# Optimization experiments

Measured on AMD Instinct MI355X. Metric: run time of the kernel, lower is better.

Reference implementation:

```python
import jax, jax.numpy as jnp
import numpy as np

B, H, W, D, R = 2, 128, 128, 128, 3   # batch, volume dims, number of SMV radii
LAM = 1e-3                            # Tikhonov term keeping the CG operator PD
EPS = 1e-12
TRUN = 10                             # truncated CG iteration count


def setup_inputs():
    key = jax.random.key(0)
    ks = jax.random.split(key, 4)
    x = jax.random.normal(ks[0], (B, H, W, D, 1), jnp.float32)
    x1 = (jax.random.uniform(ks[1], (B, H, W, D, R)) > 0.2).astype(jnp.float32)  # binary SMV masks per radius
    x3 = jax.random.uniform(ks[2], (B, H, W, D, 1), jnp.float32)        # voxelwise data weight
    init_x = jnp.zeros((B, H, W, D, 1), jnp.float32)                    # CG warm start
    smv = jax.random.uniform(ks[3], (R, H, W, D), jnp.float32)          # SMV kernels in k-space (real)
    return {"x": x, "x1": x1, "x3": x3, "init_x": init_x, "smv": smv, "trun": TRUN}


def _cg_solve(x, x1, x3, init_x, smv, trun):
    # Solve (S^H M S + lam I) u = S^H M (w3 * x) with truncated CG,
    # where S applies per-radius SMV convolution via 3D FFT and M = diag(masks).
    xv = x[..., 0]            # [B,H,W,D]
    x0 = init_x[..., 0]       # [B,H,W,D]
    w3 = x3[..., 0]           # [B,H,W,D]
    m = jnp.moveaxis(x1, -1, 1)  # [B,R,H,W,D]

    def smv_fwd(v):           # [B,H,W,D] -> [B,R,H,W,D]
        Fv = jnp.fft.fftn(v, axes=(1, 2, 3))
        return jnp.real(jnp.fft.ifftn(smv[None] * Fv[:, None], axes=(2, 3, 4)))

    def smv_adj(u):           # [B,R,H,W,D] -> [B,H,W,D] (smv real => self-adjoint kernel)
        Fu = (smv[None] * jnp.fft.fftn(u, axes=(2, 3, 4))).sum(axis=1)
        return jnp.real(jnp.fft.ifftn(Fu, axes=(1, 2, 3)))

    def A(v):
        return smv_adj(m * smv_fwd(v)) + LAM * v

    def pdot(a, b):           # per-batch inner product -> [B]
        return jnp.sum(a * b, axis=(1, 2, 3))

    b = smv_adj(m * (w3 * xv)[:, None])
    r0 = b - A(x0)

    def step(carry, _):
        xk, r, p, rs = carry
        Ap = A(p)
        alpha = (rs / (pdot(p, Ap) + EPS))[:, None, None, None]
        xk = xk + alpha * p
        r = r - alpha * Ap
        rs_new = pdot(r, r)
        beta = (rs_new / (rs + EPS))[:, None, None, None]
        p = r + beta * p
        return (xk, r, p, rs_new), None

    (xk, _, _, _), _ = jax.lax.scan(step, (x0, r0, r0, pdot(r0, r0)), None, length=trun)
    return xk[..., None]      # [B,H,W,D,1]


def reference(x, x1, x3, init_x, smv, trun):
    return _cg_solve(x, x1, x3, init_x, smv, trun)
```

## Files before the change

### kernel.cpp

```cpp
#include <hip/hip_runtime.h>

#define PI_F 3.14159265358979323846f
constexpr int VOL = 1 << 21;
constexpr float LAMBDA = 1e-3f;
constexpr int TRUNC = 10;
constexpr int LDSB = 128 * 129 * 8;

__device__ __forceinline__ float2 cmulf(float2 a, float2 b) {
    return make_float2(a.x * b.x - a.y * b.y, a.x * b.y + a.y * b.x);
}
__device__ __forceinline__ float2 cmulcf(float2 a, float2 b) {
    return make_float2(a.x * b.x + a.y * b.y, a.y * b.x - a.x * b.y);
}

template <int M>
__device__ __forceinline__ float shx(float v) {
    if constexpr (M == 1)
        return __int_as_float(__builtin_amdgcn_mov_dpp(__float_as_int(v), 0xB1, 0xF, 0xF, true));
    else if constexpr (M == 2)
        return __int_as_float(__builtin_amdgcn_mov_dpp(__float_as_int(v), 0x4E, 0xF, 0xF, true));
    else if constexpr (M == 4 || M == 8 || M == 16)
        return __int_as_float(__builtin_amdgcn_ds_swizzle(__float_as_int(v), (M << 10) | 0x1F));
    else
        return __shfl_xor(v, 32, 64);
}

__device__ __forceinline__ void plswap32(float2& a, float2& b) {
#if __has_builtin(__builtin_amdgcn_permlane32_swap)
    {
        auto rx = __builtin_amdgcn_permlane32_swap(__float_as_uint(a.x), __float_as_uint(b.x), false, false);
        a.x = __uint_as_float(rx[0]);
        b.x = __uint_as_float(rx[1]);
        auto ry = __builtin_amdgcn_permlane32_swap(__float_as_uint(a.y), __float_as_uint(b.y), false, false);
        a.y = __uint_as_float(ry[0]);
        b.y = __uint_as_float(ry[1]);
    }
#else
    {
        bool hi = (threadIdx.x & 32) != 0;
        float pax = __shfl_xor(a.x, 32, 64), pay = __shfl_xor(a.y, 32, 64);
        float pbx = __shfl_xor(b.x, 32, 64), pby = __shfl_xor(b.y, 32, 64);
        float2 na = hi ? make_float2(pbx, pby) : a;
        float2 nb = hi ? b : make_float2(pax, pay);
        a = na; b = nb;
    }
#endif
}

template <int NL>
__device__ __forceinline__ void fwd_pl32(float2 v[NL], float2 w32) {
#pragma unroll
    for (int l = 0; l < NL; l += 2) {
        plswap32(v[l], v[l + 1]);
        float2 s = make_float2(v[l].x + v[l + 1].x, v[l].y + v[l + 1].y);
        float2 d = cmulf(make_float2(v[l].x - v[l + 1].x, v[l].y - v[l + 1].y), w32);
        plswap32(s, d);
        v[l] = s;
        v[l + 1] = d;
    }
}

template <int NL>
__device__ __forceinline__ void inv_pl32(float2 v[NL], float2 w32) {
#pragma unroll
    for (int l = 0; l < NL; l += 2) {
        plswap32(v[l], v[l + 1]);
        float2 t = cmulcf(v[l + 1], w32);
        float2 s = make_float2(v[l].x + t.x, v[l].y + t.y);
        float2 d = make_float2(v[l].x - t.x, v[l].y - t.y);
        plswap32(s, d);
        v[l] = s;
        v[l + 1] = d;
    }
}

__device__ __forceinline__ void twinit2(int lane, float2 wl[6], float sg[6],
                                        float2& tw6, float2& w32) {
#pragma unroll
    for (int s = 0; s < 6; s++) {
        int m = 1 << s;
        bool hi = (lane & m) != 0;
        float ang = -PI_F * (float)(lane & (m - 1)) / (float)m;
        float sn, cs;
        __sincosf(ang, &sn, &cs);
        wl[s] = hi ? make_float2(cs, sn) : make_float2(1.f, 0.f);
        sg[s] = hi ? -1.f : 1.f;
    }
    float sn, cs;
    __sincosf(-PI_F * (float)(lane & 31) / 32.f, &sn, &cs);
    w32 = make_float2(cs, sn);
    __sincosf(-PI_F * (float)lane / 64.f, &sn, &cs);
    tw6 = make_float2(cs, sn);
}

template <int NL, int M, int S>
__device__ __forceinline__ void fwd_stage(float2 v0[NL], float2 v1[NL],
                                          const float2 wl[6], const float sg[6]) {
    const float2 w = wl[S];
    const float s = sg[S];
#pragma unroll
    for (int l = 0; l < NL; l++) {
        float2 p0 = make_float2(shx<M>(v0[l].x), shx<M>(v0[l].y));
        float2 p1 = make_float2(shx<M>(v1[l].x), shx<M>(v1[l].y));
        float2 t0 = make_float2(fmaf(v0[l].x, s, p0.x), fmaf(v0[l].y, s, p0.y));
        float2 t1 = make_float2(fmaf(v1[l].x, s, p1.x), fmaf(v1[l].y, s, p1.y));
        v0[l] = cmulf(t0, w);
        v1[l] = cmulf(t1, w);
    }
}

template <int NL, int M, int S>
__device__ __forceinline__ void inv_stage(float2 v0[NL], float2 v1[NL],
                                          const float2 wl[6], const float sg[6]) {
    const float2 w = wl[S];
    const float s = sg[S];
#pragma unroll
    for (int l = 0; l < NL; l++) {
        float2 u0 = cmulcf(v0[l], w);
        float2 u1 = cmulcf(v1[l], w);
        float2 p0 = make_float2(shx<M>(u0.x), shx<M>(u0.y));
        float2 p1 = make_float2(shx<M>(u1.x), shx<M>(u1.y));
        v0[l] = make_float2(fmaf(u0.x, s, p0.x), fmaf(u0.y, s, p0.y));
        v1[l] = make_float2(fmaf(u1.x, s, p1.x), fmaf(u1.y, s, p1.y));
    }
}

template <int NL>
__device__ __forceinline__ void fft_fwd_b(float2 v0[NL], float2 v1[NL],
                                          const float2 wl[6], const float sg[6],
                                          float2 tw6, float2 w32) {
#pragma unroll
    for (int l = 0; l < NL; l++) {
        float2 a = v0[l], b = v1[l];
        v0[l] = make_float2(a.x + b.x, a.y + b.y);
        v1[l] = cmulf(make_float2(a.x - b.x, a.y - b.y), tw6);
    }
    fwd_pl32<NL>(v0, w32);
    fwd_pl32<NL>(v1, w32);
    fwd_stage<NL, 16, 4>(v0, v1, wl, sg);
    fwd_stage<NL, 8, 3>(v0, v1, wl, sg);
    fwd_stage<NL, 4, 2>(v0, v1, wl, sg);
    fwd_stage<NL, 2, 1>(v0, v1, wl, sg);
    fwd_stage<NL, 1, 0>(v0, v1, wl, sg);
}

template <int NL>
__device__ __forceinline__ void fft_inv_b(float2 v0[NL], float2 v1[NL],
                                          const float2 wl[6], const float sg[6],
                                          float2 tw6, float2 w32) {
    inv_stage<NL, 1, 0>(v0, v1, wl, sg);
    inv_stage<NL, 2, 1>(v0, v1, wl, sg);
    inv_stage<NL, 4, 2>(v0, v1, wl, sg);
    inv_stage<NL, 8, 3>(v0, v1, wl, sg);
    inv_stage<NL, 16, 4>(v0, v1, wl, sg);
    inv_pl32<NL>(v0, w32);
    inv_pl32<NL>(v1, w32);
#pragma unroll
    for (int l = 0; l < NL; l++) {
        float2 t = cmulcf(v1[l], tw6);
        float2 n0 = make_float2(v0[l].x + t.x, v0[l].y + t.y);
        v1[l] = make_float2(v0[l].x - t.x, v0[l].y - t.y);
        v0[l] = n0;
    }
}

__device__ __forceinline__ void cg_ab(const float* scal, int i, float aP[2], float bI[2]) {
#pragma unroll
    for (int b = 0; b < 2; b++) {
        double rs = (double)scal[b], rsp = rs, a = 0.0;
        for (int k = 0; k < i; k++) {
            double pap = (double)scal[2 + 6 * k + b];
            double rap = (double)scal[4 + 6 * k + b];
            double apap = (double)scal[6 + 6 * k + b];
            a = rs / (pap + 1e-12);
            rsp = rs;
            rs = rs - 2.0 * a * rap + a * a * apap;
        }
        aP[b] = (float)a;
        bI[b] = (float)(rs / (rsp + 1e-12));
    }
}

#define PF_FWD   1
#define PF_PRE   2
#define PF_UPDP  4
#define PF_MASK  8
#define PF_LAM  16
#define PF_BOUT 32

#define LD(w_, d_) lds[(w_) * 129 + (d_)]

template <int MODE>
__global__ __launch_bounds__(1024) void k_plane(const float2* src,
                                                float2* dst,
                                                const unsigned char* __restrict__ mpk,
                                                const float2* pr,
                                                float2* pw,
                                                float2* xp,
                                                const float2* ap,
                                                float2* rw,
                                                float* __restrict__ scal, int iter) {
    extern __shared__ float2 lds[];
    __shared__ float red[6][16];
    const int t = threadIdx.x, lane = t & 63, wv = t >> 6;
    const int plane = blockIdx.x & 127;
    const int rr = blockIdx.x >> 7;
    const size_t pb = (size_t)plane * 16384;
    const size_t vb = (size_t)rr * VOL;
    float2 wl[6]; float sg[6]; float2 tw6; float2 w32;
    twinit2(lane, wl, sg, tw6, w32);

    if (MODE & PF_FWD) {
        float aP[2] = {0.f, 0.f}, bI[2] = {0.f, 0.f};
        if (MODE & PF_UPDP) cg_ab(scal, iter, aP, bI);
        float2 v0[8], v1[8];
#pragma unroll
        for (int l = 0; l < 8; l++) {
            int w = wv * 8 + l;
            size_t g = pb + (size_t)w * 128;
            if (MODE & PF_UPDP) {
                float2 r0 = rw[g + lane], r1 = rw[g + lane + 64];
                float2 p0 = pr[g + lane], p1 = pr[g + lane + 64];
                float2 A0 = ap[g + lane], A1 = ap[g + lane + 64];
                float2 X0 = xp[g + lane], X1 = xp[g + lane + 64];
                X0.x += aP[0] * p0.x; X0.y += aP[1] * p0.y;
                X1.x += aP[0] * p1.x; X1.y += aP[1] * p1.y;
                r0.x -= aP[0] * A0.x; r0.y -= aP[1] * A0.y;
                r1.x -= aP[0] * A1.x; r1.y -= aP[1] * A1.y;
                xp[g + lane] = X0; xp[g + lane + 64] = X1;
                rw[g + lane] = r0; rw[g + lane + 64] = r1;
                v0[l] = make_float2(r0.x + bI[0] * p0.x, r0.y + bI[1] * p0.y);
                v1[l] = make_float2(r1.x + bI[0] * p1.x, r1.y + bI[1] * p1.y);
                pw[g + lane] = v0[l]; pw[g + lane + 64] = v1[l];
            } else {
                v0[l] = src[g + lane];
                v1[l] = src[g + lane + 64];
                if (MODE & PF_PRE) {
                    unsigned m0 = mpk[g + lane], m1 = mpk[g + lane + 64];
                    v0[l].x *= (float)((m0 >> rr) & 1);
                    v0[l].y *= (float)((m0 >> (3 + rr)) & 1);
                    v1[l].x *= (float)((m1 >> rr) & 1);
                    v1[l].y *= (float)((m1 >> (3 + rr)) & 1);
                }
            }
        }
        fft_fwd_b<8>(v0, v1, wl, sg, tw6, w32);
#pragma unroll
        for (int l = 0; l < 8; l++) {
            int w = wv * 8 + l;
            LD(w, lane) = v0[l];
            LD(w, lane + 64) = v1[l];
        }
        __syncthreads();
#pragma unroll
        for (int l = 0; l < 8; l++) {
            int d = wv * 8 + l;
            v0[l] = LD(lane, d); v1[l] = LD(lane + 64, d);
        }
        fft_fwd_b<8>(v0, v1, wl, sg, tw6, w32);
#pragma unroll
        for (int l = 0; l < 8; l++) {
            int d = wv * 8 + l;
            LD(lane, d) = v0[l]; LD(lane + 64, d) = v1[l];
        }
        __syncthreads();
        float2* dv = dst + ((MODE & PF_PRE) ? vb : 0);
#pragma unroll
        for (int i = 0; i < 8; i++) {
            int e = t + 1024 * i;
            int w = e >> 6, d = (e & 63) * 2;
            float2 a = LD(w, d), c = LD(w, d + 1);
            *(float4*)&dv[pb + (size_t)w * 128 + d] = make_float4(a.x, a.y, c.x, c.y);
        }
    } else {
        unsigned mb0[8], mb1[8];
        if (MODE & PF_MASK) {
#pragma unroll
            for (int l = 0; l < 8; l++) {
                size_t g = pb + (size_t)(wv * 8 + l) * 128;
                mb0[l] = mpk[g + lane];
                mb1[l] = mpk[g + lane + 64];
            }
        }
        const float2* sv = src + ((MODE & PF_MASK) ? vb : 0);
#pragma unroll
        for (int i = 0; i < 8; i++) {
            int e = t + 1024 * i;
            int w = e >> 6, d = (e & 63) * 2;
            float4 f = *(const float4*)&sv[pb + (size_t)w * 128 + d];
            LD(w, d) = make_float2(f.x, f.y);
            LD(w, d + 1) = make_float2(f.z, f.w);
        }
        __syncthreads();
        float2 v0[8], v1[8];
#pragma unroll
        for (int l = 0; l < 8; l++) {
            int d = wv * 8 + l;
            v0[l] = LD(lane, d); v1[l] = LD(lane + 64, d);
        }
        fft_inv_b<8>(v0, v1, wl, sg, tw6, w32);
#pragma unroll
        for (int l = 0; l < 8; l++) {
            int d = wv * 8 + l;
            LD(lane, d) = v0[l]; LD(lane + 64, d) = v1[l];
        }
        __syncthreads();
#pragma unroll
        for (int l = 0; l < 8; l++) {
            int w = wv * 8 + l;
            v0[l] = LD(w, lane); v1[l] = LD(w, lane + 64);
        }
        fft_inv_b<8>(v0, v1, wl, sg, tw6, w32);
        float dd[6] = {0.f, 0.f, 0.f, 0.f, 0.f, 0.f};
        if (MODE & PF_MASK) {
#pragma unroll
            for (int l = 0; l < 8; l++) {
                unsigned m0 = mb0[l], m1 = mb1[l];
                v0[l].x *= (float)((m0 >> rr) & 1);
                v0[l].y *= (float)((m0 >> (3 + rr)) & 1);
                v1[l].x *= (float)((m1 >> rr) & 1);
                v1[l].y *= (float)((m1 >> (3 + rr)) & 1);
            }
            fft_fwd_b<8>(v0, v1, wl, sg, tw6, w32);
#pragma unroll
            for (int l = 0; l < 8; l++) {
                int w = wv * 8 + l;
                LD(w, lane) = v0[l];
                LD(w, lane + 64) = v1[l];
            }
            __syncthreads();
#pragma unroll
            for (int l = 0; l < 8; l++) {
                int d = wv * 8 + l;
                v0[l] = LD(lane, d); v1[l] = LD(lane + 64, d);
            }
            fft_fwd_b<8>(v0, v1, wl, sg, tw6, w32);
#pragma unroll
            for (int l = 0; l < 8; l++) {
                int d = wv * 8 + l;
                LD(lane, d) = v0[l]; LD(lane + 64, d) = v1[l];
            }
            __syncthreads();
            float2* dv = dst + vb;
#pragma unroll
            for (int i = 0; i < 8; i++) {
                int e = t + 1024 * i;
                int w = e >> 6, d = (e & 63) * 2;
                float2 a = LD(w, d), c = LD(w, d + 1);
                *(float4*)&dv[pb + (size_t)w * 128 + d] = make_float4(a.x, a.y, c.x, c.y);
            }
        } else if (MODE & PF_LAM) {
#pragma unroll
            for (int l = 0; l < 8; l++) {
                int w = wv * 8 + l;
                size_t g = pb + (size_t)w * 128;
                float2 p0 = pr[g + lane], p1 = pr[g + lane + 64];
                float2 r0 = rw[g + lane], r1 = rw[g + lane + 64];
                v0[l].x += LAMBDA * p0.x; v0[l].y += LAMBDA * p0.y;
                v1[l].x += LAMBDA * p1.x; v1[l].y += LAMBDA * p1.y;
                dst[g + lane] = v0[l];
                dst[g + lane + 64] = v1[l];
                dd[0] += p0.x * v0[l].x + p1.x * v1[l].x;
                dd[1] += p0.y * v0[l].y + p1.y * v1[l].y;
                dd[2] += r0.x * v0[l].x + r1.x * v1[l].x;
                dd[3] += r0.y * v0[l].y + r1.y * v1[l].y;
                dd[4] += v0[l].x * v0[l].x + v1[l].x * v1[l].x;
                dd[5] += v0[l].y * v0[l].y + v1[l].y * v1[l].y;
            }
        } else {
#pragma unroll
            for (int l = 0; l < 8; l++) {
                int w = wv * 8 + l;
                size_t g = pb + (size_t)w * 128;
                dst[g + lane] = v0[l];  dst[g + lane + 64] = v1[l];
                pw[g + lane] = v0[l];   pw[g + lane + 64] = v1[l];
                dd[0] += v0[l].x * v0[l].x + v1[l].x * v1[l].x;
                dd[1] += v0[l].y * v0[l].y + v1[l].y * v1[l].y;
            }
        }
        if (MODE & (PF_LAM | PF_BOUT)) {
            constexpr int ND = (MODE & PF_LAM) ? 6 : 2;
#pragma unroll
            for (int k = 0; k < ND; k++)
#pragma unroll
                for (int off = 32; off >= 1; off >>= 1)
                    dd[k] += __shfl_down(dd[k], off);
            if (lane == 0)
#pragma unroll
                for (int k = 0; k < ND; k++) red[k][wv] = dd[k];
            __syncthreads();
            if (t == 0) {
                const int base = (MODE & PF_BOUT) ? 0 : 2 + 6 * iter;
#pragma unroll
                for (int k = 0; k < ND; k++) {
                    float s = 0.f;
#pragma unroll
                    for (int i = 0; i < 16; i++) s += red[k][i];
                    atomicAdd(&scal[base + k], s);
                }
            }
        }
    }
}

__global__ __launch_bounds__(256) void k_hspread(const float2* __restrict__ Vs,
                                                 float2* __restrict__ T,
                                                 const float* __restrict__ sEt) {
    __shared__ float2 lds[128][17];
    const int t = threadIdx.x, lane = t & 63, wv = t >> 6;
    const int w = blockIdx.x >> 3;
    const int d0 = (blockIdx.x & 7) * 16;
    float2 wl[6]; float sg[6]; float2 tw6; float2 w32;
    twinit2(lane, wl, sg, tw6, w32);
#pragma unroll
    for (int i = 0; i < 4; i++) {
        int e = t + 256 * i;
        int h = e >> 3, f = e & 7;
        float4 v = *(const float4*)&Vs[(size_t)h * 16384 + w * 128 + d0 + f * 2];
        lds[h][f * 2] = make_float2(v.x, v.y);
        lds[h][f * 2 + 1] = make_float2(v.z, v.w);
    }
    __syncthreads();
    float2 s0[4], s1[4];
#pragma unroll
    for (int q = 0; q < 4; q++) {
        int dd = wv * 4 + q;
        s0[q] = lds[lane][dd];
        s1[q] = lds[lane + 64][dd];
    }
    fft_fwd_b<4>(s0, s1, wl, sg, tw6, w32);
    for (int r = 0; r < 3; r++) {
        __syncthreads();
        float2 u0[4], u1[4];
#pragma unroll
        for (int q = 0; q < 4; q++) {
            int dd = wv * 4 + q;
            size_t sb = (size_t)r * VOL + (size_t)w * 16384 + (size_t)(d0 + dd) * 128;
            float e0 = sEt[sb + lane], e1 = sEt[sb + lane + 64];
            u0[q] = make_float2(s0[q].x * e0, s0[q].y * e0);
            u1[q] = make_float2(s1[q].x * e1, s1[q].y * e1);
        }
        fft_inv_b<4>(u0, u1, wl, sg, tw6, w32);
#pragma unroll
        for (int q = 0; q < 4; q++) {
            int dd = wv * 4 + q;
            lds[lane][dd] = u0[q];
            lds[lane + 64][dd] = u1[q];
        }
        __syncthreads();
        float2* Tr = T + (size_t)r * VOL;
#pragma unroll
        for (int i = 0; i < 4; i++) {
            int e = t + 256 * i;
            int h = e >> 3, f = e & 7;
            float2 a = lds[h][f * 2], b = lds[h][f * 2 + 1];
            *(float4*)&Tr[(size_t)h * 16384 + w * 128 + d0 + f * 2] =
                make_float4(a.x, a.y, b.x, b.y);
        }
    }
}

__global__ __launch_bounds__(256) void k_hadj(const float2* __restrict__ T,
                                              float2* __restrict__ Wv,
                                              const float* __restrict__ sEt) {
    __shared__ float2 lds[128][17];
    const int t = threadIdx.x, lane = t & 63, wv = t >> 6;
    const int w = blockIdx.x >> 3;
    const int d0 = (blockIdx.x & 7) * 16;
    float2 wl[6]; float sg[6]; float2 tw6; float2 w32;
    twinit2(lane, wl, sg, tw6, w32);
    float2 a0[4], a1[4];
#pragma unroll
    for (int q = 0; q < 4; q++) {
        a0[q] = make_float2(0.f, 0.f);
        a1[q] = make_float2(0.f, 0.f);
    }
    for (int r = 0; r < 3; r++) {
        if (r) __syncthreads();
        const float2* Tr = T + (size_t)r * VOL;
#pragma unroll
        for (int i = 0; i < 4; i++) {
            int e = t + 256 * i;
            int h = e >> 3, f = e & 7;
            float4 v = *(const float4*)&Tr[(size_t)h * 16384 + w * 128 + d0 + f * 2];
            lds[h][f * 2] = make_float2(v.x, v.y);
            lds[h][f * 2 + 1] = make_float2(v.z, v.w);
        }
        __syncthreads();
        float2 v0[4], v1[4];
#pragma unroll
        for (int q = 0; q < 4; q++) {
            int dd = wv * 4 + q;
            v0[q] = lds[lane][dd];
            v1[q] = lds[lane + 64][dd];
        }
        fft_fwd_b<4>(v0, v1, wl, sg, tw6, w32);
#pragma unroll
        for (int q = 0; q < 4; q++) {
            int dd = wv * 4 + q;
            size_t sb = (size_t)r * VOL + (size_t)w * 16384 + (size_t)(d0 + dd) * 128;
            float e0 = sEt[sb + lane], e1 = sEt[sb + lane + 64];
            a0[q].x += v0[q].x * e0; a0[q].y += v0[q].y * e0;
            a1[q].x += v1[q].x * e1; a1[q].y += v1[q].y * e1;
        }
    }
    __syncthreads();
    fft_inv_b<4>(a0, a1, wl, sg, tw6, w32);
#pragma unroll
    for (int q = 0; q < 4; q++) {
        int dd = wv * 4 + q;
        lds[lane][dd] = a0[q];
        lds[lane + 64][dd] = a1[q];
    }
    __syncthreads();
#pragma unroll
    for (int i = 0; i < 4; i++) {
        int e = t + 256 * i;
        int h = e >> 3, f = e & 7;
        float2 a = lds[h][f * 2], b = lds[h][f * 2 + 1];
        *(float4*)&Wv[(size_t)h * 16384 + w * 128 + d0 + f * 2] =
            make_float4(a.x, a.y, b.x, b.y);
    }
}

__global__ void k_sE(const float* __restrict__ smv, float* __restrict__ sEt) {
    int j = blockIdx.x * 256 + threadIdx.x;
    int w = j >> 14, d = (j >> 7) & 127, h = j & 127;
    int kh = __brev(h) >> 25, kw = __brev(w) >> 25, kd = __brev(d) >> 25;
    int nh = (128 - kh) & 127, nw = (128 - kw) & 127, nd = (128 - kd) & 127;
    const float sc = 0.5f / 2097152.0f;
#pragma unroll
    for (int r = 0; r < 3; r++) {
        const float* s = smv + (size_t)r * VOL;
        float a = s[(kh << 14) | (kw << 7) | kd];
        float b = s[(nh << 14) | (nw << 7) | nd];
        sEt[(size_t)r * VOL + j] = (a + b) * sc;
    }
}

__global__ void k_packm(const float* __restrict__ x1, unsigned char* __restrict__ mpk) {
    int j = blockIdx.x * 256 + threadIdx.x;
    unsigned b = 0;
#pragma unroll
    for (int r = 0; r < 3; r++) {
        b |= (x1[(size_t)j * 3 + r] != 0.f ? 1u : 0u) << r;
        b |= (x1[((size_t)VOL + j) * 3 + r] != 0.f ? 1u : 0u) << (3 + r);
    }
    mpk[j] = (unsigned char)b;
}

__global__ void k_packt(const float* __restrict__ x, const float* __restrict__ x3,
                        float2* __restrict__ t) {
    int j = blockIdx.x * 256 + threadIdx.x;
    t[j] = make_float2(x[j] * x3[j], x[VOL + j] * x3[VOL + j]);
}

__global__ void k_packx(const float* __restrict__ ix, float2* __restrict__ xv) {
    int j = blockIdx.x * 256 + threadIdx.x;
    xv[j] = make_float2(ix[j], ix[VOL + j]);
}

__global__ void k_zero(float* __restrict__ scal) {
    if (threadIdx.x < 64) scal[threadIdx.x] = 0.0f;
}

__global__ void k_fin(float* __restrict__ scal) {
    if (threadIdx.x < 2) {
        int b = threadIdx.x;
        double rs = (double)scal[b];
        for (int k = 0; k < TRUNC - 1; k++) {
            double pap = (double)scal[2 + 6 * k + b];
            double rap = (double)scal[4 + 6 * k + b];
            double apap = (double)scal[6 + 6 * k + b];
            double a = rs / (pap + 1e-12);
            rs = rs - 2.0 * a * rap + a * a * apap;
        }
        scal[62 + b] = (float)(rs / ((double)scal[2 + 6 * (TRUNC - 1) + b] + 1e-12));
    }
}

__global__ void k_unpackf(const float2* __restrict__ x, const float2* __restrict__ p,
                          const float* __restrict__ scal, float* __restrict__ out) {
    int j = blockIdx.x * 256 + threadIdx.x;
    float a0 = scal[62], a1 = scal[63];
    float2 xv = x[j], pv = p[j];
    out[j] = xv.x + a0 * pv.x;
    out[VOL + j] = xv.y + a1 * pv.y;
}

constexpr int M_FWD    = PF_FWD;
constexpr int M_FWDP   = PF_FWD | PF_UPDP;
constexpr int M_FWDPRE = PF_FWD | PF_PRE;
constexpr int M_MASK   = PF_MASK;
constexpr int M_LAM    = PF_LAM;
constexpr int M_BOUT   = PF_BOUT;

extern "C" void kernel_launch(void* const* d_in, const int* in_sizes, int n_in,
                              void* d_out, int out_size, void* d_ws, size_t ws_size,
                              hipStream_t stream) {
    const float* x   = (const float*)d_in[0];
    const float* x1  = (const float*)d_in[1];
    const float* x3  = (const float*)d_in[2];
    const float* ix  = (const float*)d_in[3];
    const float* smv = (const float*)d_in[4];
    float* out = (float*)d_out;

    hipFuncSetAttribute((const void*)k_plane<M_FWD>,    hipFuncAttributeMaxDynamicSharedMemorySize, LDSB);
    hipFuncSetAttribute((const void*)k_plane<M_FWDP>,   hipFuncAttributeMaxDynamicSharedMemorySize, LDSB);
    hipFuncSetAttribute((const void*)k_plane<M_FWDPRE>, hipFuncAttributeMaxDynamicSharedMemorySize, LDSB);
    hipFuncSetAttribute((const void*)k_plane<M_MASK>,   hipFuncAttributeMaxDynamicSharedMemorySize, LDSB);
    hipFuncSetAttribute((const void*)k_plane<M_LAM>,    hipFuncAttributeMaxDynamicSharedMemorySize, LDSB);
    hipFuncSetAttribute((const void*)k_plane<M_BOUT>,   hipFuncAttributeMaxDynamicSharedMemorySize, LDSB);

    char* ws = (char*)d_ws;
    size_t off = 0;
    auto alloc = [&](size_t bytes) {
        void* p = ws + off;
        off += (bytes + 255) & ~(size_t)255;
        return p;
    };
    float*  sEt = (float*)alloc((size_t)3 * VOL * 4);
    unsigned char* mpk = (unsigned char*)alloc((size_t)VOL);
    float2* tp  = (float2*)alloc((size_t)VOL * 8);
    float2* xv  = (float2*)alloc((size_t)VOL * 8);
    float2* rv  = (float2*)alloc((size_t)VOL * 8);
    float2* pv  = (float2*)alloc((size_t)VOL * 8);
    float2* Ap  = (float2*)alloc((size_t)VOL * 8);
    float2* Vs  = (float2*)alloc((size_t)VOL * 8);
    float2* T   = (float2*)alloc((size_t)3 * VOL * 8);
    float2* W   = (float2*)alloc((size_t)VOL * 8);
    float*  scal = (float*)alloc(256);

    const int GE = VOL / 256;

    k_zero<<<1, 64, 0, stream>>>(scal);
    k_sE<<<GE, 256, 0, stream>>>(smv, sEt);
    k_packm<<<GE, 256, 0, stream>>>(x1, mpk);
    k_packt<<<GE, 256, 0, stream>>>(x, x3, tp);
    k_packx<<<GE, 256, 0, stream>>>(ix, xv);

    k_plane<M_FWDPRE><<<384, 1024, LDSB, stream>>>(tp, T, mpk, nullptr, nullptr, nullptr, nullptr, nullptr, nullptr, 0);
    k_hadj<<<1024, 256, 0, stream>>>(T, W, sEt);
    k_plane<M_BOUT><<<128, 1024, LDSB, stream>>>(W, rv, nullptr, nullptr, pv, nullptr, nullptr, nullptr, scal, 0);

    for (int i = 0; i < TRUNC; i++) {
        if (i == 0)
            k_plane<M_FWD><<<128, 1024, LDSB, stream>>>(pv, Vs, nullptr, nullptr, nullptr, nullptr, nullptr, nullptr, nullptr, 0);
        else
            k_plane<M_FWDP><<<128, 1024, LDSB, stream>>>(nullptr, Vs, nullptr, pv, pv, xv, Ap, rv, scal, i);
        k_hspread<<<1024, 256, 0, stream>>>(Vs, T, sEt);
        k_plane<M_MASK><<<384, 1024, LDSB, stream>>>(T, T, mpk, nullptr, nullptr, nullptr, nullptr, nullptr, nullptr, 0);
        k_hadj<<<1024, 256, 0, stream>>>(T, W, sEt);
        k_plane<M_LAM><<<128, 1024, LDSB, stream>>>(W, Ap, nullptr, pv, nullptr, nullptr, nullptr, rv, scal, i);
    }

    k_fin<<<1, 64, 0, stream>>>(scal);
    k_unpackf<<<GE, 256, 0, stream>>>(xv, pv, scal, out);
    (void)in_sizes; (void)n_in; (void)out_size; (void)ws_size;
}
```

Measured before the change: 1.899 ms.

## Split plane FFT transpose into two half-width LDS passes to halve shared memory

```diff
diff --git a/kernel.cpp b/kernel.cpp
--- a/kernel.cpp
+++ b/kernel.cpp
@@ -4,7 +4,8 @@
 constexpr int VOL = 1 << 21;
 constexpr float LAMBDA = 1e-3f;
 constexpr int TRUNC = 10;
-constexpr int LDSB = 128 * 129 * 8;
+constexpr int LDSB  = 128 * 129 * 8;
+constexpr int LDSB2 = 128 * 65 * 8;
 
 __device__ __forceinline__ float2 cmulf(float2 a, float2 b) {
     return make_float2(a.x * b.x - a.y * b.y, a.x * b.y + a.y * b.x);
@@ -403,6 +404,127 @@
     }
 }
 
+#define LH(w_, c_) lds[(w_) * 65 + (c_)]
+
+__device__ __forceinline__ void h_fwd_half(float2* lds, float2* dv, size_t pb,
+                                           const float2 vh[8], int dof,
+                                           int t, int lane, int wv,
+                                           const float2 wl[6], const float sg[6],
+                                           float2 tw6, float2 w32) {
+    __syncthreads();
+#pragma unroll
+    for (int l = 0; l < 8; l++) LH(wv * 8 + l, lane) = vh[l];
+    __syncthreads();
+    float2 u0[4], u1[4];
+#pragma unroll
+    for (int q = 0; q < 4; q++) {
+        int c = wv * 4 + q;
+        u0[q] = LH(lane, c); u1[q] = LH(lane + 64, c);
+    }
+    fft_fwd_b<4>(u0, u1, wl, sg, tw6, w32);
+#pragma unroll
+    for (int q = 0; q < 4; q++) {
+        int c = wv * 4 + q;
+        LH(lane, c) = u0[q]; LH(lane + 64, c) = u1[q];
+    }
+    __syncthreads();
+#pragma unroll
+    for (int i = 0; i < 4; i++) {
+        int e = t + 1024 * i;
+        int w = e >> 5, d = (e & 31) * 2;
+        float2 a = LH(w, d), b = LH(w, d + 1);
+        *(float4*)&dv[pb + (size_t)w * 128 + dof + d] = make_float4(a.x, a.y, b.x, b.y);
+    }
+}
+
+__device__ __forceinline__ void h_inv_half(float2* lds, const float2* sv, size_t pb,
+                                           float2 vh[8], int dof,
+                                           int t, int lane, int wv,
+                                           const float2 wl[6], const float sg[6],
+                                           float2 tw6, float2 w32) {
+    __syncthreads();
+#pragma unroll
+    for (int i = 0; i < 4; i++) {
+        int e = t + 1024 * i;
+        int w = e >> 5, d = (e & 31) * 2;
+        float4 f = *(const float4*)&sv[pb + (size_t)w * 128 + dof + d];
+        LH(w, d) = make_float2(f.x, f.y);
+        LH(w, d + 1) = make_float2(f.z, f.w);
+    }
+    __syncthreads();
+    float2 u0[4], u1[4];
+#pragma unroll
+    for (int q = 0; q < 4; q++) {
+        int c = wv * 4 + q;
+        u0[q] = LH(lane, c); u1[q] = LH(lane + 64, c);
+    }
+    fft_inv_b<4>(u0, u1, wl, sg, tw6, w32);
+#pragma unroll
+    for (int q = 0; q < 4; q++) {
+        int c = wv * 4 + q;
+        LH(lane, c) = u0[q]; LH(lane + 64, c) = u1[q];
+    }
+    __syncthreads();
+#pragma unroll
+    for (int l = 0; l < 8; l++) vh[l] = LH(wv * 8 + l, lane);
+}
+
+template <int MODE>
+__global__ __launch_bounds__(1024) void k_plane2(const float2* src,
+                                                 float2* dst,
+                                                 const unsigned char* __restrict__ mpk) {
+    extern __shared__ float2 lds[];
+    const int t = threadIdx.x, lane = t & 63, wv = t >> 6;
+    const int plane = blockIdx.x & 127;
+    const int rr = blockIdx.x >> 7;
+    const size_t pb = (size_t)plane * 16384;
+    const size_t vb = (size_t)rr * VOL;
+    float2 wl[6]; float sg[6]; float2 tw6; float2 w32;
+    twinit2(lane, wl, sg, tw6, w32);
+    float2 v0[8], v1[8];
+
+    if (MODE & PF_FWD) {
+#pragma unroll
+        for (int l = 0; l < 8; l++) {
+            int w = wv * 8 + l;
+            size_t g = pb + (size_t)w * 128;
+            v0[l] = src[g + lane];
+            v1[l] = src[g + lane + 64];
+            unsigned m0 = mpk[g + lane], m1 = mpk[g + lane + 64];
+            v0[l].x *= (float)((m0 >> rr) & 1);
+            v0[l].y *= (float)((m0 >> (3 + rr)) & 1);
+            v1[l].x *= (float)((m1 >> rr) & 1);
+            v1[l].y *= (float)((m1 >> (3 + rr)) & 1);
+        }
+        fft_fwd_b<8>(v0, v1, wl, sg, tw6, w32);
+        h_fwd_half(lds, dst + vb, pb, v0, 0, t, lane, wv, wl, sg, tw6, w32);
+        h_fwd_half(lds, dst + vb, pb, v1, 64, t, lane, wv, wl, sg, tw6, w32);
+    } else {
+        unsigned pk0 = 0, pk1 = 0;
+#pragma unroll
+        for (int l = 0; l < 8; l++) {
+            size_t g = pb + (size_t)(wv * 8 + l) * 128;
+            unsigned m0 = mpk[g + lane], m1 = mpk[g + lane + 64];
+            pk0 |= (((m0 >> rr) & 1) | (((m0 >> (3 + rr)) & 1) << 1)) << (2 * l);
+            pk1 |= (((m1 >> rr) & 1) | (((m1 >> (3 + rr)) & 1) << 1)) << (2 * l);
+        }
+        const float2* sv = src + vb;
+        h_inv_half(lds, sv, pb, v0, 0, t, lane, wv, wl, sg, tw6, w32);
+        h_inv_half(lds, sv, pb, v1, 64, t, lane, wv, wl, sg, tw6, w32);
+        fft_inv_b<8>(v0, v1, wl, sg, tw6, w32);
+#pragma unroll
+        for (int l = 0; l < 8; l++) {
+            v0[l].x *= (float)((pk0 >> (2 * l)) & 1);
+            v0[l].y *= (float)((pk0 >> (2 * l + 1)) & 1);
+            v1[l].x *= (float)((pk1 >> (2 * l)) & 1);
+            v1[l].y *= (float)((pk1 >> (2 * l + 1)) & 1);
+        }
+        fft_fwd_b<8>(v0, v1, wl, sg, tw6, w32);
+        h_fwd_half(lds, dst + vb, pb, v0, 0, t, lane, wv, wl, sg, tw6, w32);
+        h_fwd_half(lds, dst + vb, pb, v1, 64, t, lane, wv, wl, sg, tw6, w32);
+    }
+}
+
 __global__ __launch_bounds__(256) void k_hspread(const float2* __restrict__ Vs,
                                                  float2* __restrict__ T,
                                                  const float* __restrict__ sEt) {
@@ -590,10 +712,10 @@
 
 constexpr int M_FWD    = PF_FWD;
 constexpr int M_FWDP   = PF_FWD | PF_UPDP;
-constexpr int M_FWDPRE = PF_FWD | PF_PRE;
-constexpr int M_MASK   = PF_MASK;
 constexpr int M_LAM    = PF_LAM;
 constexpr int M_BOUT   = PF_BOUT;
+constexpr int M_MASK2  = PF_MASK;
+constexpr int M_PRE2   = PF_FWD | PF_PRE;
 
 extern "C" void kernel_launch(void* const* d_in, const int* in_sizes, int n_in,
                               void* d_out, int out_size, void* d_ws, size_t ws_size,
@@ -607,10 +729,10 @@
 
     hipFuncSetAttribute((const void*)k_plane<M_FWD>,    hipFuncAttributeMaxDynamicSharedMemorySize, LDSB);
     hipFuncSetAttribute((const void*)k_plane<M_FWDP>,   hipFuncAttributeMaxDynamicSharedMemorySize, LDSB);
-    hipFuncSetAttribute((const void*)k_plane<M_FWDPRE>, hipFuncAttributeMaxDynamicSharedMemorySize, LDSB);
-    hipFuncSetAttribute((const void*)k_plane<M_MASK>,   hipFuncAttributeMaxDynamicSharedMemorySize, LDSB);
     hipFuncSetAttribute((const void*)k_plane<M_LAM>,    hipFuncAttributeMaxDynamicSharedMemorySize, LDSB);
     hipFuncSetAttribute((const void*)k_plane<M_BOUT>,   hipFuncAttributeMaxDynamicSharedMemorySize, LDSB);
+    hipFuncSetAttribute((const void*)k_plane2<M_MASK2>, hipFuncAttributeMaxDynamicSharedMemorySize, LDSB2);
+    hipFuncSetAttribute((const void*)k_plane2<M_PRE2>,  hipFuncAttributeMaxDynamicSharedMemorySize, LDSB2);
 
     char* ws = (char*)d_ws;
     size_t off = 0;
@@ -639,7 +761,7 @@
     k_packt<<<GE, 256, 0, stream>>>(x, x3, tp);
     k_packx<<<GE, 256, 0, stream>>>(ix, xv);
 
-    k_plane<M_FWDPRE><<<384, 1024, LDSB, stream>>>(tp, T, mpk, nullptr, nullptr, nullptr, nullptr, nullptr, nullptr, 0);
+    k_plane2<M_PRE2><<<384, 1024, LDSB2, stream>>>(tp, T, mpk);
     k_hadj<<<1024, 256, 0, stream>>>(T, W, sEt);
     k_plane<M_BOUT><<<128, 1024, LDSB, stream>>>(W, rv, nullptr, nullptr, pv, nullptr, nullptr, nullptr, scal, 0);
 
@@ -649,7 +771,7 @@
         else
             k_plane<M_FWDP><<<128, 1024, LDSB, stream>>>(nullptr, Vs, nullptr, pv, pv, xv, Ap, rv, scal, i);
         k_hspread<<<1024, 256, 0, stream>>>(Vs, T, sEt);
-        k_plane<M_MASK><<<384, 1024, LDSB, stream>>>(T, T, mpk, nullptr, nullptr, nullptr, nullptr, nullptr, nullptr, 0);
+        k_plane2<M_MASK2><<<384, 1024, LDSB2, stream>>>(T, T, mpk);
         k_hadj<<<1024, 256, 0, stream>>>(T, W, sEt);
         k_plane<M_LAM><<<128, 1024, LDSB, stream>>>(W, Ap, nullptr, pv, nullptr, nullptr, nullptr, rv, scal, i);
     }
```

New measurement: 2.108 ms. +11.0%, slower.
